# Performance work log

Hardware: AMD Instinct MI355X
Metric: run time of the kernel (lower is better)

The kernel has to match this reference:

```python
import jax, jax.numpy as jnp
import numpy as np

N_NODES = 100000
N_EDGES = 1600000
F_IN = 256
HID = 256
N_CLS = 40


def _glorot(key, shape):
    lim = float(np.sqrt(6.0 / (shape[0] + shape[1])))
    return jax.random.uniform(key, shape, jnp.float32, -lim, lim)


def setup_inputs() -> dict:
    key = jax.random.key(0)
    ks = jax.random.split(key, 8)
    x = jax.random.normal(ks[0], (N_NODES, F_IN), jnp.float32)
    edge_index = jax.random.randint(ks[1], (2, N_EDGES), 0, N_NODES, jnp.int64)
    return {
        "x": x,
        "edge_index": edge_index,
        "W1": _glorot(ks[2], (F_IN, HID)),
        "b1": jnp.zeros((HID,), jnp.float32),
        "W2": _glorot(ks[3], (HID, HID)),
        "b2": jnp.zeros((HID,), jnp.float32),
        "W3": _glorot(ks[4], (HID, N_CLS)),
        "b3": jnp.zeros((N_CLS,), jnp.float32),
    }


def _gcn_conv(x, W, b, src, dst, norm, num_nodes):
    # linear transform first (PyG GCNConv), then normalized scatter-add
    h = x @ W                                   # [N, out]
    msg = h[src] * norm[:, None]                # [E+N, out] gathered messages
    out = jax.ops.segment_sum(msg, dst, num_segments=num_nodes)
    return out + b


def reference(x, edge_index, W1, b1, W2, b2, W3, b3):
    n = x.shape[0]
    loop = jnp.arange(n, dtype=edge_index.dtype)
    src = jnp.concatenate([edge_index[0], loop])  # add self-loops
    dst = jnp.concatenate([edge_index[1], loop])
    # symmetric GCN normalization: deg^{-1/2}[src] * deg^{-1/2}[dst]
    deg = jax.ops.segment_sum(jnp.ones_like(dst, dtype=x.dtype), dst, num_segments=n)
    dinv = jnp.where(deg > 0, jax.lax.rsqrt(deg), 0.0)
    norm = dinv[src] * dinv[dst]

    h = jax.nn.relu(_gcn_conv(x, W1, b1, src, dst, norm, n))  # dropout p=0.0 is identity
    h = jax.nn.relu(_gcn_conv(h, W2, b2, src, dst, norm, n))
    out = _gcn_conv(h, W3, b3, src, dst, norm, n)             # logits [N, num_classes]
    return out
```

## Files before the change

kernel.cpp:

```cpp
#include <hip/hip_runtime.h>
#include <hip/hip_bf16.h>
#include <cstdint>
#include <cstddef>

#define NNODES 100000
#define NEDGES 1600000
#define NCLS 40
#define NBLK_SCAN 391
#define NBUCK 391
#define BCAP 5120
#define NBLKB 256
#define CHUNK 6250
#define MPAD 100096

typedef _Float16 f16;
typedef _Float16 f16x8 __attribute__((ext_vector_type(8)));
typedef float f32x4 __attribute__((ext_vector_type(4)));

__device__ inline float h2f(unsigned short u) {
    f16 h; __builtin_memcpy(&h, &u, 2); return (float)h;
}
__device__ inline unsigned short f2h(float f) {
    f16 h = (f16)f; unsigned short u; __builtin_memcpy(&u, &h, 2); return u;
}
__device__ inline void gload_lds16(const void* g, void* l) {
    __builtin_amdgcn_global_load_lds((const __attribute__((address_space(1))) unsigned int*)g,
                                     (__attribute__((address_space(3))) unsigned int*)l, 16, 0, 0);
}
__device__ inline void fmix2(float& alo, float& ahi, unsigned u, float one) {
    asm("v_fma_mix_f32 %0, %1, %2, %0 op_sel:[0,0,0] op_sel_hi:[1,0,0]"
        : "+v"(alo) : "v"(u), "v"(one));
    asm("v_fma_mix_f32 %0, %1, %2, %0 op_sel:[1,0,0] op_sel_hi:[1,0,0]"
        : "+v"(ahi) : "v"(u), "v"(one));
}

__global__ void k_detect(const int* __restrict__ ei, int* __restrict__ flag, int* __restrict__ gbcnt) {
    const int t = threadIdx.x;
    for (int i = t; i < NBUCK; i += 64) gbcnt[i] = 0;
    if (t == 0) {
        int nz = 0;
        for (int i = 1; i < 256; i += 2) nz |= ei[i];
        *flag = (nz == 0) ? 1 : 0;
    }
}

__global__ __launch_bounds__(256) void k_bucket(const int* __restrict__ ei,
        const int* __restrict__ flag, int* __restrict__ gbcnt, int2* __restrict__ bedge) {
    __shared__ int lcnt[NBUCK], lbase[NBUCK], lcur[NBUCK];
    const int t = threadIdx.x;
    const int is64 = *flag;
    for (int i = t; i < NBUCK; i += 256) lcnt[i] = 0;
    __syncthreads();
    const int e0 = blockIdx.x * CHUNK;
    for (int i = t; i < CHUNK; i += 256) {
        int e = e0 + i;
        int d = is64 ? ei[2 * ((size_t)NEDGES + e)] : ei[NEDGES + e];
        atomicAdd(&lcnt[d >> 8], 1);
    }
    __syncthreads();
    for (int i = t; i < NBUCK; i += 256) {
        int c = lcnt[i];
        lbase[i] = c ? atomicAdd(&gbcnt[i], c) : 0;
        lcur[i] = 0;
    }
    __syncthreads();
    for (int i = t; i < CHUNK; i += 256) {
        int e = e0 + i;
        int s, d;
        if (is64) { s = ei[2 * (size_t)e]; d = ei[2 * ((size_t)NEDGES + e)]; }
        else      { s = ei[e];             d = ei[NEDGES + e]; }
        int b = d >> 8;
        int p = lbase[b] + atomicAdd(&lcur[b], 1);
        if (p < BCAP) bedge[(size_t)b * BCAP + p] = make_int2(s, d);
    }
}

__global__ __launch_bounds__(256) void k_cnt(const int* __restrict__ gbcnt,
        const int2* __restrict__ bedge, int* __restrict__ cnt) {
    __shared__ int lc[256];
    const int t = threadIdx.x, b = blockIdx.x;
    lc[t] = 0;
    __syncthreads();
    const int ne = min(gbcnt[b], BCAP);
    const int2* be = bedge + (size_t)b * BCAP;
    for (int i = t; i < ne; i += 256)
        atomicAdd(&lc[be[i].y & 255], 1);
    __syncthreads();
    int node = b * 256 + t;
    if (node < NNODES) cnt[node] = lc[t];
}

__global__ __launch_bounds__(256) void k_scan1(const int* __restrict__ cnt,
        int* __restrict__ incl, int* __restrict__ blksum, float* __restrict__ dinv) {
    __shared__ int sm[256];
    const int t = threadIdx.x;
    int i = blockIdx.x * 256 + t;
    int cv = (i < NNODES) ? cnt[i] : 0;
    dinv[i] = (i < NNODES) ? rsqrtf((float)(cv + 1)) : 0.f;
    int v = (i < NNODES) ? (cv + 1) : 0;
    sm[t] = v;
    __syncthreads();
    for (int d = 1; d < 256; d <<= 1) {
        int x = (t >= d) ? sm[t - d] : 0;
        __syncthreads();
        sm[t] += x;
        __syncthreads();
    }
    if (i < NNODES) incl[i] = sm[t];
    if (t == 255) blksum[blockIdx.x] = sm[255];
}

__global__ __launch_bounds__(512) void k_scan2(const int* __restrict__ blksum, int* __restrict__ blkoff) {
    __shared__ int sm[512];
    const int t = threadIdx.x;
    int v = (t < NBLK_SCAN) ? blksum[t] : 0;
    sm[t] = v;
    __syncthreads();
    for (int d = 1; d < 512; d <<= 1) {
        int x = (t >= d) ? sm[t - d] : 0;
        __syncthreads();
        sm[t] += x;
        __syncthreads();
    }
    if (t < NBLK_SCAN) blkoff[t] = sm[t] - v;
}

__global__ __launch_bounds__(256) void k_scan3(const int* __restrict__ incl,
        const int* __restrict__ blkoff, const int* __restrict__ cnt,
        int* __restrict__ offs, int* __restrict__ esrc) {
    int i = blockIdx.x * 256 + threadIdx.x;
    if (i < NNODES) {
        int o1 = incl[i] + blkoff[blockIdx.x];
        offs[i + 1] = o1;
        esrc[o1 - (cnt[i] + 1)] = i;
    }
    if (i == 0) offs[0] = 0;
}

__global__ __launch_bounds__(256) void k_fill2(const int* __restrict__ gbcnt,
        const int2* __restrict__ bedge, const int* __restrict__ offs, int* __restrict__ esrc) {
    __shared__ int loff[256], lcur[256];
    const int t = threadIdx.x, b = blockIdx.x;
    int node = b * 256 + t;
    loff[t] = (node < NNODES) ? offs[node] : 0;
    lcur[t] = 0;
    __syncthreads();
    const int ne = min(gbcnt[b], BCAP);
    const int2* be = bedge + (size_t)b * BCAP;
    for (int i = t; i < ne; i += 256) {
        int2 sd = be[i];
        int li = sd.y & 255;
        int p = loff[li] + 1 + atomicAdd(&lcur[li], 1);
        esrc[p] = sd.x;
    }
}

__global__ __launch_bounds__(256) void k_wts(const float* __restrict__ W1, const float* __restrict__ W2,
        const float* __restrict__ W3, unsigned short* __restrict__ W1T,
        unsigned short* __restrict__ W2T, unsigned short* __restrict__ W3T) {
    const int b = blockIdx.x, n = threadIdx.x;
    if (b < 256) {
        W1T[n * 256 + b] = f2h(W1[b * 256 + n]);
    } else if (b < 512) {
        int k = b - 256;
        W2T[n * 256 + k] = f2h(W2[k * 256 + n]);
    } else {
        int nn = b - 512;
        W3T[nn * 256 + n] = (nn < NCLS) ? f2h(W3[n * NCLS + nn]) : (unsigned short)0;
    }
}

template<bool A32, bool NARROW>
__global__ __launch_bounds__(256) void gemm_core(const void* __restrict__ Ap,
        const unsigned short* __restrict__ BT, unsigned short* __restrict__ C,
        const float* __restrict__ dinv) {
    __shared__ __align__(16) char lds[65536];
    const int t = threadIdx.x;
    const int w = t >> 6, l = t & 63;
    const int bm = blockIdx.x * 128;
    const int bn = blockIdx.y * 128;
    const int lr = l >> 3, ls = l & 7;
    const unsigned short* A16 = (const unsigned short*)Ap;
    const float* A32p = (const float*)Ap;

    auto stageB = [&](int buf, int k0) {
        char* base = lds + buf * 32768 + 16384;
#pragma unroll
        for (int i = 0; i < 4; ++i) {
            int r = w * 32 + i * 8 + lr;
            int sl = ls ^ (r & 7);
            const char* gB = (const char*)BT + (size_t)(bn + r) * 512 + (size_t)k0 * 2 + sl * 16;
            gload_lds16(gB, base + (w * 32 + i * 8) * 128);
        }
    };
    auto stageA16 = [&](int buf, int k0) {
        char* base = lds + buf * 32768;
#pragma unroll
        for (int i = 0; i < 4; ++i) {
            int r = w * 32 + i * 8 + lr;
            int sl = ls ^ (r & 7);
            const char* gA = (const char*)A16 + (size_t)(bm + r) * 512 + (size_t)k0 * 2 + sl * 16;
            gload_lds16(gA, base + (w * 32 + i * 8) * 128);
        }
    };
    float4 areg[8];
    auto issueA32 = [&](int k0) {
#pragma unroll
        for (int i = 0; i < 8; ++i) {
            int tt = i * 256 + t;
            int r = tt >> 4, q = tt & 15;
            float4 v = make_float4(0.f, 0.f, 0.f, 0.f);
            if (bm + r < NNODES) v = *(const float4*)(A32p + (size_t)(bm + r) * 256 + k0 + q * 4);
            areg[i] = v;
        }
    };
    auto writeA32 = [&](int buf) {
        char* base = lds + buf * 32768;
#pragma unroll
        for (int i = 0; i < 8; ++i) {
            int tt = i * 256 + t;
            int r = tt >> 4, q = tt & 15;
            f16 h4[4] = {(f16)areg[i].x, (f16)areg[i].y, (f16)areg[i].z, (f16)areg[i].w};
            char* dst = base + r * 128 + (((q >> 1) ^ (r & 7)) * 16) + (q & 1) * 8;
            __builtin_memcpy(dst, h4, 8);
        }
    };

    f32x4 acc[4][4];
#pragma unroll
    for (int m = 0; m < 4; ++m)
#pragma unroll
        for (int n = 0; n < 4; ++n)
            acc[m][n] = (f32x4){0.f, 0.f, 0.f, 0.f};

    const int frow = l & 15, fk = l >> 4;
    const int r0w = (w >> 1) * 64, c0w = (w & 1) * 64;

    if constexpr (A32) { issueA32(0); } else { stageA16(0, 0); }
    stageB(0, 0);
    if constexpr (A32) { writeA32(0); }
    __syncthreads();
    for (int kt = 0; kt < 4; ++kt) {
        const int buf = kt & 1;
        if (kt < 3) {
            if constexpr (A32) { issueA32((kt + 1) * 64); } else { stageA16(buf ^ 1, (kt + 1) * 64); }
            stageB(buf ^ 1, (kt + 1) * 64);
        }
        const char* As = lds + buf * 32768;
        const char* Bs = As + 16384;
#pragma unroll
        for (int ks = 0; ks < 2; ++ks) {
            f16x8 af[4], bf[4];
#pragma unroll
            for (int m = 0; m < 4; ++m) {
                int ra = r0w + m * 16 + frow;
                af[m] = *(const f16x8*)(As + ra * 128 + (((ks * 4 + fk) ^ (ra & 7)) * 16));
            }
#pragma unroll
            for (int n = 0; n < 4; ++n) {
                int rb = c0w + n * 16 + frow;
                bf[n] = *(const f16x8*)(Bs + rb * 128 + (((ks * 4 + fk) ^ (rb & 7)) * 16));
            }
#pragma unroll
            for (int m = 0; m < 4; ++m)
#pragma unroll
                for (int n = 0; n < 4; ++n)
                    acc[m][n] = __builtin_amdgcn_mfma_f32_16x16x32_f16(af[m], bf[n], acc[m][n], 0, 0, 0);
        }
        if constexpr (A32) { if (kt < 3) writeA32(buf ^ 1); }
        __syncthreads();
    }

    unsigned short* Cs = (unsigned short*)lds;
    const int crow = (l >> 4) * 4, ccol = l & 15;
#pragma unroll
    for (int m = 0; m < 4; ++m) {
        float4 dv = *(const float4*)(dinv + bm + r0w + m * 16 + crow);
        float d4[4] = {dv.x, dv.y, dv.z, dv.w};
#pragma unroll
        for (int n = 0; n < 4; ++n)
#pragma unroll
            for (int r = 0; r < 4; ++r)
                Cs[(r0w + m * 16 + crow + r) * 136 + c0w + n * 16 + ccol] = f2h(acc[m][n][r] * d4[r]);
    }
    __syncthreads();
#pragma unroll
    for (int i = 0; i < 8; ++i) {
        int row = i * 16 + (t >> 4);
        int cs = t & 15;
        uint4 v = *(const uint4*)(Cs + row * 136 + cs * 8);
        if constexpr (NARROW) {
            if (cs < 5)
                *(uint4*)((char*)C + (size_t)(bm + row) * 80 + cs * 16) = v;
        } else {
            *(uint4*)((char*)C + (size_t)(bm + row) * 512 + bn * 2 + cs * 16) = v;
        }
    }
}

__global__ __launch_bounds__(256) void agg_v3(const unsigned short* __restrict__ T,
        const int* __restrict__ esrc, const int* __restrict__ offs,
        const float* __restrict__ dinv, const float* __restrict__ bias,
        unsigned short* __restrict__ outh) {
    int node = blockIdx.x * 4 + (threadIdx.x >> 6);
    if (node >= NNODES) return;
    const int l = threadIdx.x & 63;
    const float one = 1.0f;
    const int e0 = offs[node], e1 = offs[node + 1];
    const int ne = e1 - e0;
    const int myidx = esrc[e0 + min(l, ne - 1)];
    const char* Tb = (const char*)T;
    float a0 = 0.f, a1 = 0.f, a2 = 0.f, a3 = 0.f;
    const int nreg = min(ne, 64);
    int j = 0;
    for (; j + 8 <= nreg; j += 8) {
        uint2 u[8];
#pragma unroll
        for (int q = 0; q < 8; ++q) {
            int s = __builtin_amdgcn_readlane(myidx, j + q);
            u[q] = *(const uint2*)(Tb + (size_t)s * 512 + l * 8);
        }
#pragma unroll
        for (int q = 0; q < 8; ++q) {
            fmix2(a0, a1, u[q].x, one);
            fmix2(a2, a3, u[q].y, one);
        }
    }
    for (; j < nreg; ++j) {
        int s = __builtin_amdgcn_readlane(myidx, j);
        uint2 u = *(const uint2*)(Tb + (size_t)s * 512 + l * 8);
        fmix2(a0, a1, u.x, one);
        fmix2(a2, a3, u.y, one);
    }
    for (int e = e0 + 64; e < e1; ++e) {
        int s = esrc[e];
        uint2 u = *(const uint2*)(Tb + (size_t)s * 512 + l * 8);
        fmix2(a0, a1, u.x, one);
        fmix2(a2, a3, u.y, one);
    }
    float di = dinv[node];
    float4 bv = *(const float4*)(bias + l * 4);
    float r0 = fmaxf(fmaf(a0, di, bv.x), 0.f);
    float r1 = fmaxf(fmaf(a1, di, bv.y), 0.f);
    float r2 = fmaxf(fmaf(a2, di, bv.z), 0.f);
    float r3 = fmaxf(fmaf(a3, di, bv.w), 0.f);
    uint2 o;
    o.x = (unsigned)f2h(r0) | ((unsigned)f2h(r1) << 16);
    o.y = (unsigned)f2h(r2) | ((unsigned)f2h(r3) << 16);
    *(uint2*)(outh + (size_t)node * 256 + l * 4) = o;
}

__global__ __launch_bounds__(256) void agg_out_v3(const unsigned short* __restrict__ T,
        const int* __restrict__ esrc, const int* __restrict__ offs,
        const float* __restrict__ dinv, const float* __restrict__ bias,
        float* __restrict__ out) {
    int node = blockIdx.x * 4 + (threadIdx.x >> 6);
    if (node >= NNODES) return;
    const int l = threadIdx.x & 63;
    const int g = l >> 4, sl = l & 15;
    const bool act = sl < 10;
    const float one = 1.0f;
    const int e0 = offs[node], e1 = offs[node + 1];
    const int ne = e1 - e0;
    const int myidx = esrc[e0 + min(l, ne - 1)];
    const int nreg = min(ne, 64);
    const char* Tb = (const char*)T;
    float a0 = 0.f, a1 = 0.f, a2 = 0.f, a3 = 0.f;
    for (int j = 0; j < nreg; j += 4) {
        int jj = j + g;
        int s = __shfl(myidx, min(jj, 63), 64);
        if (jj < nreg && act) {
            uint2 u = *(const uint2*)(Tb + (size_t)s * 80 + sl * 8);
            fmix2(a0, a1, u.x, one);
            fmix2(a2, a3, u.y, one);
        }
    }
    for (int e = e0 + 64 + g; e < e1; e += 4) {
        int s = esrc[e];
        if (act) {
            uint2 u = *(const uint2*)(Tb + (size_t)s * 80 + sl * 8);
            fmix2(a0, a1, u.x, one);
            fmix2(a2, a3, u.y, one);
        }
    }
    a0 += __shfl_xor(a0, 16, 64); a1 += __shfl_xor(a1, 16, 64);
    a2 += __shfl_xor(a2, 16, 64); a3 += __shfl_xor(a3, 16, 64);
    a0 += __shfl_xor(a0, 32, 64); a1 += __shfl_xor(a1, 32, 64);
    a2 += __shfl_xor(a2, 32, 64); a3 += __shfl_xor(a3, 32, 64);
    if (g == 0 && act) {
        float di = dinv[node];
        float4 bv = *(const float4*)(bias + sl * 4);
        float4 o = make_float4(fmaf(a0, di, bv.x), fmaf(a1, di, bv.y),
                               fmaf(a2, di, bv.z), fmaf(a3, di, bv.w));
        *(float4*)(out + (size_t)node * 40 + sl * 4) = o;
    }
}

extern "C" void kernel_launch(void* const* d_in, const int* in_sizes, int n_in,
                              void* d_out, int out_size, void* d_ws, size_t ws_size,
                              hipStream_t stream) {
    const float* x  = (const float*)d_in[0];
    const int*   ei = (const int*)d_in[1];
    const float* W1 = (const float*)d_in[2];
    const float* b1 = (const float*)d_in[3];
    const float* W2 = (const float*)d_in[4];
    const float* b2 = (const float*)d_in[5];
    const float* W3 = (const float*)d_in[6];
    const float* b3 = (const float*)d_in[7];
    float* out = (float*)d_out;

    char* ws = (char*)d_ws;
    size_t o = 0;
    unsigned short* tbA  = (unsigned short*)(ws + o); o += (size_t)MPAD * 256 * 2;
    unsigned short* tbB  = (unsigned short*)(ws + o); o += (size_t)MPAD * 256 * 2;
    unsigned short* tb40 = (unsigned short*)(ws + o); o += (size_t)MPAD * NCLS * 2;
    unsigned short* W1T  = (unsigned short*)(ws + o); o += 131072;
    unsigned short* W2T  = (unsigned short*)(ws + o); o += 131072;
    unsigned short* W3T  = (unsigned short*)(ws + o); o += 65536;
    int2* bedge  = (int2*)(ws + o);  o += (size_t)NBUCK * BCAP * 8;
    int* gbcnt   = (int*)(ws + o);   o += 2048;
    int* esrc    = (int*)(ws + o);   o += (size_t)(NEDGES + NNODES) * 4;
    int* cnt     = (int*)(ws + o);   o += 400128;
    int* offs    = (int*)(ws + o);   o += 400384;
    float* dinv  = (float*)(ws + o); o += 400384;
    int* incl    = (int*)(ws + o);   o += 400128;
    int* blksum  = (int*)(ws + o);   o += 2048;
    int* blkoff  = (int*)(ws + o);   o += 2048;
    int* flag    = (int*)(ws + o);   o += 256;
    if (ws_size < o) return;

    hipMemsetAsync(tbB + (size_t)NNODES * 256, 0, (MPAD - NNODES) * 512, stream);

    k_detect<<<1, 64, 0, stream>>>(ei, flag, gbcnt);
    k_bucket<<<NBLKB, 256, 0, stream>>>(ei, flag, gbcnt, bedge);
    k_cnt<<<NBUCK, 256, 0, stream>>>(gbcnt, bedge, cnt);
    k_scan1<<<NBLK_SCAN, 256, 0, stream>>>(cnt, incl, blksum, dinv);
    k_scan2<<<1, 512, 0, stream>>>(blksum, blkoff);
    k_scan3<<<NBLK_SCAN, 256, 0, stream>>>(incl, blkoff, cnt, offs, esrc);
    k_fill2<<<NBUCK, 256, 0, stream>>>(gbcnt, bedge, offs, esrc);

    k_wts<<<640, 256, 0, stream>>>(W1, W2, W3, W1T, W2T, W3T);

    dim3 gg(MPAD / 128, 2), b256(256);
    gemm_core<true, false><<<gg, b256, 0, stream>>>(x, W1T, tbA, dinv);
    agg_v3<<<NNODES / 4, 256, 0, stream>>>(tbA, esrc, offs, dinv, b1, tbB);
    gemm_core<false, false><<<gg, b256, 0, stream>>>(tbB, W2T, tbA, dinv);
    agg_v3<<<NNODES / 4, 256, 0, stream>>>(tbA, esrc, offs, dinv, b2, tbB);
    gemm_core<false, true><<<dim3(MPAD / 128, 1), b256, 0, stream>>>(tbB, W3T, tb40, dinv);
    agg_out_v3<<<NNODES / 4, 256, 0, stream>>>(tb40, esrc, offs, dinv, b3, out);
}
```

Measured before the change: 478.9 us.

## Use full-width 64x256 GEMM tiles, split bucket edge storage, fold setup kernels

The hidden-layer GEMMs now use 64-row by 256-column tiles, so each block computes every output column and the A matrix (including the fp32 input x) is read only once instead of twice across a 2-wide column grid. The edge bucket buffer is split into a 4-byte source array and a 1-byte local destination array, which cuts bytes moved in the counting and fill passes. The detect kernel, the padding memset and the weight transpose are merged into a single launch. The GEMM blocks now use 80KB of LDS, which may lower occupancy, and the grid has more, smaller blocks.

```diff
diff --git a/kernel.cpp b/kernel.cpp
--- a/kernel.cpp
+++ b/kernel.cpp
@@ -34,18 +34,35 @@
         : "+v"(ahi) : "v"(u), "v"(one));
 }
 
-__global__ void k_detect(const int* __restrict__ ei, int* __restrict__ flag, int* __restrict__ gbcnt) {
-    const int t = threadIdx.x;
-    for (int i = t; i < NBUCK; i += 64) gbcnt[i] = 0;
-    if (t == 0) {
-        int nz = 0;
-        for (int i = 1; i < 256; i += 2) nz |= ei[i];
-        *flag = (nz == 0) ? 1 : 0;
+__global__ __launch_bounds__(256) void k_wts(const float* __restrict__ W1, const float* __restrict__ W2,
+        const float* __restrict__ W3, unsigned short* __restrict__ W1T,
+        unsigned short* __restrict__ W2T, unsigned short* __restrict__ W3T,
+        unsigned short* __restrict__ tbBpad, const int* __restrict__ ei,
+        int* __restrict__ flag, int* __restrict__ gbcnt) {
+    const int b = blockIdx.x, n = threadIdx.x;
+    if (b < 256) {
+        W1T[n * 256 + b] = f2h(W1[b * 256 + n]);
+    } else if (b < 512) {
+        int k = b - 256;
+        W2T[n * 256 + k] = f2h(W2[k * 256 + n]);
+    } else if (b < 640) {
+        int nn = b - 512;
+        W3T[nn * 256 + n] = (nn < NCLS) ? f2h(W3[n * NCLS + nn]) : (unsigned short)0;
+        int idx = nn * 256 + n;
+        if (idx < (MPAD - NNODES) * 256) tbBpad[idx] = 0;
+    } else {
+        for (int i = n; i < NBUCK; i += 256) gbcnt[i] = 0;
+        if (n == 0) {
+            int nz = 0;
+            for (int i = 1; i < 256; i += 2) nz |= ei[i];
+            *flag = (nz == 0) ? 1 : 0;
+        }
     }
 }
 
 __global__ __launch_bounds__(256) void k_bucket(const int* __restrict__ ei,
-        const int* __restrict__ flag, int* __restrict__ gbcnt, int2* __restrict__ bedge) {
+        const int* __restrict__ flag, int* __restrict__ gbcnt,
+        int* __restrict__ bsrc, unsigned char* __restrict__ bdst8) {
     __shared__ int lcnt[NBUCK], lbase[NBUCK], lcur[NBUCK];
     const int t = threadIdx.x;
     const int is64 = *flag;
@@ -71,20 +88,23 @@
         else      { s = ei[e];             d = ei[NEDGES + e]; }
         int b = d >> 8;
         int p = lbase[b] + atomicAdd(&lcur[b], 1);
-        if (p < BCAP) bedge[(size_t)b * BCAP + p] = make_int2(s, d);
+        if (p < BCAP) {
+            bsrc[(size_t)b * BCAP + p] = s;
+            bdst8[(size_t)b * BCAP + p] = (unsigned char)(d & 255);
+        }
     }
 }
 
 __global__ __launch_bounds__(256) void k_cnt(const int* __restrict__ gbcnt,
-        const int2* __restrict__ bedge, int* __restrict__ cnt) {
+        const unsigned char* __restrict__ bdst8, int* __restrict__ cnt) {
     __shared__ int lc[256];
     const int t = threadIdx.x, b = blockIdx.x;
     lc[t] = 0;
     __syncthreads();
     const int ne = min(gbcnt[b], BCAP);
-    const int2* be = bedge + (size_t)b * BCAP;
+    const unsigned char* bd = bdst8 + (size_t)b * BCAP;
     for (int i = t; i < ne; i += 256)
-        atomicAdd(&lc[be[i].y & 255], 1);
+        atomicAdd(&lc[bd[i]], 1);
     __syncthreads();
     int node = b * 256 + t;
     if (node < NNODES) cnt[node] = lc[t];
@@ -138,7 +158,8 @@
 }
 
 __global__ __launch_bounds__(256) void k_fill2(const int* __restrict__ gbcnt,
-        const int2* __restrict__ bedge, const int* __restrict__ offs, int* __restrict__ esrc) {
+        const int* __restrict__ bsrc, const unsigned char* __restrict__ bdst8,
+        const int* __restrict__ offs, int* __restrict__ esrc) {
     __shared__ int loff[256], lcur[256];
     const int t = threadIdx.x, b = blockIdx.x;
     int node = b * 256 + t;
@@ -146,54 +167,149 @@
     lcur[t] = 0;
     __syncthreads();
     const int ne = min(gbcnt[b], BCAP);
-    const int2* be = bedge + (size_t)b * BCAP;
+    const int* bs = bsrc + (size_t)b * BCAP;
+    const unsigned char* bd = bdst8 + (size_t)b * BCAP;
     for (int i = t; i < ne; i += 256) {
-        int2 sd = be[i];
-        int li = sd.y & 255;
+        int s = bs[i];
+        int li = bd[i];
         int p = loff[li] + 1 + atomicAdd(&lcur[li], 1);
-        esrc[p] = sd.x;
-    }
-}
-
-__global__ __launch_bounds__(256) void k_wts(const float* __restrict__ W1, const float* __restrict__ W2,
-        const float* __restrict__ W3, unsigned short* __restrict__ W1T,
-        unsigned short* __restrict__ W2T, unsigned short* __restrict__ W3T) {
-    const int b = blockIdx.x, n = threadIdx.x;
-    if (b < 256) {
-        W1T[n * 256 + b] = f2h(W1[b * 256 + n]);
-    } else if (b < 512) {
-        int k = b - 256;
-        W2T[n * 256 + k] = f2h(W2[k * 256 + n]);
-    } else {
-        int nn = b - 512;
-        W3T[nn * 256 + n] = (nn < NCLS) ? f2h(W3[n * NCLS + nn]) : (unsigned short)0;
-    }
-}
-
-template<bool A32, bool NARROW>
-__global__ __launch_bounds__(256) void gemm_core(const void* __restrict__ Ap,
+        esrc[p] = s;
+    }
+}
+
+template<bool A32>
+__global__ __launch_bounds__(256) void gemm_w(const void* __restrict__ Ap,
+        const unsigned short* __restrict__ BT, unsigned short* __restrict__ C,
+        const float* __restrict__ dinv) {
+    __shared__ __align__(16) char lds[81920];
+    const int t = threadIdx.x;
+    const int w = t >> 6, l = t & 63;
+    const int bm = blockIdx.x * 64;
+    const int lr = l >> 3, ls = l & 7;
+    const unsigned short* A16 = (const unsigned short*)Ap;
+    const float* A32p = (const float*)Ap;
+
+    auto stageB = [&](int buf, int k0) {
+        char* base = lds + buf * 40960 + 8192;
+#pragma unroll
+        for (int i = 0; i < 8; ++i) {
+            int r = w * 64 + i * 8 + lr;
+            int sl = ls ^ (r & 7);
+            const char* gB = (const char*)BT + (size_t)r * 512 + (size_t)k0 * 2 + sl * 16;
+            gload_lds16(gB, base + (w * 64 + i * 8) * 128);
+        }
+    };
+    auto stageA16 = [&](int buf, int k0) {
+        char* base = lds + buf * 40960;
+#pragma unroll
+        for (int i = 0; i < 2; ++i) {
+            int r = w * 16 + i * 8 + lr;
+            int sl = ls ^ (r & 7);
+            const char* gA = (const char*)A16 + (size_t)(bm + r) * 512 + (size_t)k0 * 2 + sl * 16;
+            gload_lds16(gA, base + (w * 16 + i * 8) * 128);
+        }
+    };
+    float4 areg[4];
+    const int arow = t >> 2, akq = (t & 3) << 4;
+    auto issueA32 = [&](int k0) {
+#pragma unroll
+        for (int i = 0; i < 4; ++i) {
+            float4 v = make_float4(0.f, 0.f, 0.f, 0.f);
+            if (bm + arow < NNODES) v = *(const float4*)(A32p + (size_t)(bm + arow) * 256 + k0 + akq + i * 4);
+            areg[i] = v;
+        }
+    };
+    auto writeA32 = [&](int buf) {
+        char* base = lds + buf * 40960;
+        f16 h[16];
+#pragma unroll
+        for (int i = 0; i < 4; ++i) {
+            h[i * 4 + 0] = (f16)areg[i].x; h[i * 4 + 1] = (f16)areg[i].y;
+            h[i * 4 + 2] = (f16)areg[i].z; h[i * 4 + 3] = (f16)areg[i].w;
+        }
+        int s0 = (t & 3) * 2;
+        char* d0 = base + arow * 128 + ((s0 ^ (arow & 7)) * 16);
+        char* d1 = base + arow * 128 + (((s0 + 1) ^ (arow & 7)) * 16);
+        __builtin_memcpy(d0, &h[0], 16);
+        __builtin_memcpy(d1, &h[8], 16);
+    };
+
+    f32x4 acc[4][4];
+#pragma unroll
+    for (int m = 0; m < 4; ++m)
+#pragma unroll
+        for (int n = 0; n < 4; ++n)
+            acc[m][n] = (f32x4){0.f, 0.f, 0.f, 0.f};
+
+    const int frow = l & 15, fk = l >> 4;
+
+    if constexpr (A32) { issueA32(0); } else { stageA16(0, 0); }
+    stageB(0, 0);
+    if constexpr (A32) { writeA32(0); }
+    __syncthreads();
+    for (int kt = 0; kt < 4; ++kt) {
+        const int buf = kt & 1;
+        if (kt < 3) {
+            if constexpr (A32) { issueA32((kt + 1) * 64); } else { stageA16(buf ^ 1, (kt + 1) * 64); }
+            stageB(buf ^ 1, (kt + 1) * 64);
+        }
+        const char* As = lds + buf * 40960;
+        const char* Bs = As + 8192;
+#pragma unroll
+        for (int ks = 0; ks < 2; ++ks) {
+            f16x8 af[4], bf[4];
+#pragma unroll
+            for (int m = 0; m < 4; ++m) {
+                int ra = m * 16 + frow;
+                af[m] = *(const f16x8*)(As + ra * 128 + (((ks * 4 + fk) ^ (ra & 7)) * 16));
+            }
+#pragma unroll
+            for (int n = 0; n < 4; ++n) {
+                int rb = w * 64 + n * 16 + frow;
+                bf[n] = *(const f16x8*)(Bs + rb * 128 + (((ks * 4 + fk) ^ (rb & 7)) * 16));
+            }
+#pragma unroll
+            for (int m = 0; m < 4; ++m)
+#pragma unroll
+                for (int n = 0; n < 4; ++n)
+                    acc[m][n] = __builtin_amdgcn_mfma_f32_16x16x32_f16(af[m], bf[n], acc[m][n], 0, 0, 0);
+        }
+        if constexpr (A32) { if (kt < 3) writeA32(buf ^ 1); }
+        __syncthreads();
+    }
+
+    unsigned short* Cs = (unsigned short*)lds;
+    const int crow = (l >> 4) * 4, ccol = l & 15;
+#pragma unroll
+    for (int m = 0; m < 4; ++m) {
+        float4 dv = *(const float4*)(dinv + bm + m * 16 + crow);
+        float d4[4] = {dv.x, dv.y, dv.z, dv.w};
+#pragma unroll
+        for (int n = 0; n < 4; ++n)
+#pragma unroll
+            for (int r = 0; r < 4; ++r)
+                Cs[(m * 16 + crow + r) * 264 + w * 64 + n * 16 + ccol] = f2h(acc[m][n][r] * d4[r]);
+    }
+    __syncthreads();
+#pragma unroll
+    for (int i = 0; i < 8; ++i) {
+        int idx = i * 256 + t;
+        int row = idx >> 5, cs = idx & 31;
+        uint4 v = *(const uint4*)(Cs + row * 264 + cs * 8);
+        *(uint4*)((char*)C + (size_t)(bm + row) * 512 + cs * 16) = v;
+    }
+}
+
+__global__ __launch_bounds__(256) void gemm_n(const unsigned short* __restrict__ A16,
         const unsigned short* __restrict__ BT, unsigned short* __restrict__ C,
         const float* __restrict__ dinv) {
     __shared__ __align__(16) char lds[65536];
     const int t = threadIdx.x;
     const int w = t >> 6, l = t & 63;
     const int bm = blockIdx.x * 128;
-    const int bn = blockIdx.y * 128;
     const int lr = l >> 3, ls = l & 7;
-    const unsigned short* A16 = (const unsigned short*)Ap;
-    const float* A32p = (const float*)Ap;
-
-    auto stageB = [&](int buf, int k0) {
-        char* base = lds + buf * 32768 + 16384;
-#pragma unroll
-        for (int i = 0; i < 4; ++i) {
-            int r = w * 32 + i * 8 + lr;
-            int sl = ls ^ (r & 7);
-            const char* gB = (const char*)BT + (size_t)(bn + r) * 512 + (size_t)k0 * 2 + sl * 16;
-            gload_lds16(gB, base + (w * 32 + i * 8) * 128);
-        }
-    };
-    auto stageA16 = [&](int buf, int k0) {
+
+    auto stage = [&](int buf, int k0) {
         char* base = lds + buf * 32768;
 #pragma unroll
         for (int i = 0; i < 4; ++i) {
@@ -201,28 +317,8 @@
             int sl = ls ^ (r & 7);
             const char* gA = (const char*)A16 + (size_t)(bm + r) * 512 + (size_t)k0 * 2 + sl * 16;
             gload_lds16(gA, base + (w * 32 + i * 8) * 128);
-        }
-    };
-    float4 areg[8];
-    auto issueA32 = [&](int k0) {
-#pragma unroll
-        for (int i = 0; i < 8; ++i) {
-            int tt = i * 256 + t;
-            int r = tt >> 4, q = tt & 15;
-            float4 v = make_float4(0.f, 0.f, 0.f, 0.f);
-            if (bm + r < NNODES) v = *(const float4*)(A32p + (size_t)(bm + r) * 256 + k0 + q * 4);
-            areg[i] = v;
-        }
-    };
-    auto writeA32 = [&](int buf) {
-        char* base = lds + buf * 32768;
-#pragma unroll
-        for (int i = 0; i < 8; ++i) {
-            int tt = i * 256 + t;
-            int r = tt >> 4, q = tt & 15;
-            f16 h4[4] = {(f16)areg[i].x, (f16)areg[i].y, (f16)areg[i].z, (f16)areg[i].w};
-            char* dst = base + r * 128 + (((q >> 1) ^ (r & 7)) * 16) + (q & 1) * 8;
-            __builtin_memcpy(dst, h4, 8);
+            const char* gB = (const char*)BT + (size_t)r * 512 + (size_t)k0 * 2 + sl * 16;
+            gload_lds16(gB, base + 16384 + (w * 32 + i * 8) * 128);
         }
     };
 
@@ -236,16 +332,11 @@
     const int frow = l & 15, fk = l >> 4;
     const int r0w = (w >> 1) * 64, c0w = (w & 1) * 64;
 
-    if constexpr (A32) { issueA32(0); } else { stageA16(0, 0); }
-    stageB(0, 0);
-    if constexpr (A32) { writeA32(0); }
+    stage(0, 0);
     __syncthreads();
     for (int kt = 0; kt < 4; ++kt) {
         const int buf = kt & 1;
-        if (kt < 3) {
-            if constexpr (A32) { issueA32((kt + 1) * 64); } else { stageA16(buf ^ 1, (kt + 1) * 64); }
-            stageB(buf ^ 1, (kt + 1) * 64);
-        }
+        if (kt < 3) stage(buf ^ 1, (kt + 1) * 64);
         const char* As = lds + buf * 32768;
         const char* Bs = As + 16384;
 #pragma unroll
@@ -267,7 +358,6 @@
                 for (int n = 0; n < 4; ++n)
                     acc[m][n] = __builtin_amdgcn_mfma_f32_16x16x32_f16(af[m], bf[n], acc[m][n], 0, 0, 0);
         }
-        if constexpr (A32) { if (kt < 3) writeA32(buf ^ 1); }
         __syncthreads();
     }
 
@@ -288,12 +378,9 @@
     for (int i = 0; i < 8; ++i) {
         int row = i * 16 + (t >> 4);
         int cs = t & 15;
-        uint4 v = *(const uint4*)(Cs + row * 136 + cs * 8);
-        if constexpr (NARROW) {
-            if (cs < 5)
-                *(uint4*)((char*)C + (size_t)(bm + row) * 80 + cs * 16) = v;
-        } else {
-            *(uint4*)((char*)C + (size_t)(bm + row) * 512 + bn * 2 + cs * 16) = v;
+        if (cs < 5) {
+            uint4 v = *(const uint4*)(Cs + row * 136 + cs * 8);
+            *(uint4*)((char*)C + (size_t)(bm + row) * 80 + cs * 16) = v;
         }
     }
 }
@@ -417,7 +504,8 @@
     unsigned short* W1T  = (unsigned short*)(ws + o); o += 131072;
     unsigned short* W2T  = (unsigned short*)(ws + o); o += 131072;
     unsigned short* W3T  = (unsigned short*)(ws + o); o += 65536;
-    int2* bedge  = (int2*)(ws + o);  o += (size_t)NBUCK * BCAP * 8;
+    int* bsrc    = (int*)(ws + o);   o += (size_t)NBUCK * BCAP * 4;
+    unsigned char* bdst8 = (unsigned char*)(ws + o); o += (size_t)NBUCK * BCAP + 256;
     int* gbcnt   = (int*)(ws + o);   o += 2048;
     int* esrc    = (int*)(ws + o);   o += (size_t)(NEDGES + NNODES) * 4;
     int* cnt     = (int*)(ws + o);   o += 400128;
@@ -429,23 +517,20 @@
     int* flag    = (int*)(ws + o);   o += 256;
     if (ws_size < o) return;
 
-    hipMemsetAsync(tbB + (size_t)NNODES * 256, 0, (MPAD - NNODES) * 512, stream);
-
-    k_detect<<<1, 64, 0, stream>>>(ei, flag, gbcnt);
-    k_bucket<<<NBLKB, 256, 0, stream>>>(ei, flag, gbcnt, bedge);
-    k_cnt<<<NBUCK, 256, 0, stream>>>(gbcnt, bedge, cnt);
+    k_wts<<<641, 256, 0, stream>>>(W1, W2, W3, W1T, W2T, W3T,
+                                   tbB + (size_t)NNODES * 256, ei, flag, gbcnt);
+    k_bucket<<<NBLKB, 256, 0, stream>>>(ei, flag, gbcnt, bsrc, bdst8);
+    k_cnt<<<NBUCK, 256, 0, stream>>>(gbcnt, bdst8, cnt);
     k_scan1<<<NBLK_SCAN, 256, 0, stream>>>(cnt, incl, blksum, dinv);
     k_scan2<<<1, 512, 0, stream>>>(blksum, blkoff);
     k_scan3<<<NBLK_SCAN, 256, 0, stream>>>(incl, blkoff, cnt, offs, esrc);
-    k_fill2<<<NBUCK, 256, 0, stream>>>(gbcnt, bedge, offs, esrc);
-
-    k_wts<<<640, 256, 0, stream>>>(W1, W2, W3, W1T, W2T, W3T);
-
-    dim3 gg(MPAD / 128, 2), b256(256);
-    gemm_core<true, false><<<gg, b256, 0, stream>>>(x, W1T, tbA, dinv);
+    k_fill2<<<NBUCK, 256, 0, stream>>>(gbcnt, bsrc, bdst8, offs, esrc);
+
+    dim3 b256(256);
+    gemm_w<true><<<MPAD / 64, b256, 0, stream>>>(x, W1T, tbA, dinv);
     agg_v3<<<NNODES / 4, 256, 0, stream>>>(tbA, esrc, offs, dinv, b1, tbB);
-    gemm_core<false, false><<<gg, b256, 0, stream>>>(tbB, W2T, tbA, dinv);
+    gemm_w<false><<<MPAD / 64, b256, 0, stream>>>(tbB, W2T, tbA, dinv);
     agg_v3<<<NNODES / 4, 256, 0, stream>>>(tbA, esrc, offs, dinv, b2, tbB);
-    gemm_core<false, true><<<dim3(MPAD / 128, 1), b256, 0, stream>>>(tbB, W3T, tb40, dinv);
+    gemm_n<<<MPAD / 128, b256, 0, stream>>>(tbB, W3T, tb40, dinv);
     agg_out_v3<<<NNODES / 4, 256, 0, stream>>>(tb40, esrc, offs, dinv, b3, out);
 }
```

Result: faster. 459.5 us (-4.0%).
